# Kernel tuning notes

Hardware: AMD Instinct MI355X
Metric: run time of the kernel (lower is better)

The kernel has to match this reference:

```python
import jax, jax.numpy as jnp
import numpy as np

B, S, D, H = 4, 2048, 256, 8
DH = D // H  # d_head = 32


def setup_inputs() -> dict:
    key = jax.random.key(0)
    ks = jax.random.split(key, 7)
    scale = 1.0 / np.sqrt(D)  # ~ torch Linear init range
    sequences = jax.random.normal(ks[0], (B, S, D), dtype=jnp.float32)
    Wq = jax.random.uniform(ks[1], (H, D, DH), jnp.float32, -scale, scale)
    Wk = jax.random.uniform(ks[2], (H, D, DH), jnp.float32, -scale, scale)
    Wv = jax.random.uniform(ks[3], (H, D, DH), jnp.float32, -scale, scale)
    bq = jax.random.uniform(ks[4], (H, DH), jnp.float32, -scale, scale)
    bk = jax.random.uniform(ks[5], (H, DH), jnp.float32, -scale, scale)
    bv = jax.random.uniform(ks[6], (H, DH), jnp.float32, -scale, scale)
    return {"sequences": sequences, "Wq": Wq, "Wk": Wk, "Wv": Wv,
            "bq": bq, "bk": bk, "bv": bv}


def reference(sequences, Wq, Wk, Wv, bq, bk, bv):
    # Per-head linear maps of the FULL token (use_linear_mapping=True):
    # q[b,h,s,e] = sequences[b,s,:] @ Wq[h] + bq[h]
    q = jnp.einsum('bsd,hde->bhse', sequences, Wq) + bq[None, :, None, :]
    k = jnp.einsum('bsd,hde->bhse', sequences, Wk) + bk[None, :, None, :]
    v = jnp.einsum('bsd,hde->bhse', sequences, Wv) + bv[None, :, None, :]
    # Scaled dot-product attention per batch/head (full SxS matrix, as original)
    scores = jnp.einsum('bhse,bhte->bhst', q, k) / jnp.sqrt(jnp.float32(DH))
    attn = jax.nn.softmax(scores, axis=-1)
    out = jnp.einsum('bhst,bhte->bhse', attn, v)
    # hstack heads along feature dim -> [B, S, D]
    return out.transpose(0, 2, 1, 3).reshape(B, S, D)
```

## Files before the change

### kernel.cpp

```cpp
#include <hip/hip_runtime.h>
#include <hip/hip_bf16.h>


#define NB 4
#define NS 2048
#define ND 256
#define NH 8
#define NDH 32
#define KT 128
#define NT (NS / KT)

typedef __attribute__((ext_vector_type(8))) short short8;
typedef __attribute__((ext_vector_type(4))) float float4v;

static __device__ __forceinline__ unsigned short f2bf(float f) {
    union { float f; unsigned int u; } v; v.f = f;
    unsigned int r = (v.u + 0x7FFFu + ((v.u >> 16) & 1u)) >> 16;
    return (unsigned short)r;
}

static __device__ __forceinline__ unsigned int pk2bf(float lo, float hi) {
    __hip_bfloat162 h = __float22bfloat162_rn(float2{lo, hi});
    union { __hip_bfloat162 h; unsigned int u; } c; c.h = h;
    return c.u;
}

#if defined(__has_builtin)
#if __has_builtin(__builtin_amdgcn_exp2f)
#define EXP2F(x) __builtin_amdgcn_exp2f(x)
#endif
#endif
#ifndef EXP2F
#define EXP2F(x) exp2f(x)
#endif

#define SWZ(x) ((x) ^ ((((x) >> 7) & 7) << 4))

__global__ __launch_bounds__(256) void prep(const float* __restrict__ seq,
                                            unsigned short* __restrict__ seqb,
                                            const float* __restrict__ Wq,
                                            const float* __restrict__ Wk,
                                            const float* __restrict__ Wv,
                                            unsigned short* __restrict__ Wt) {
    int bx = (int)blockIdx.x;
    if (bx < 2048) {
        int i = (bx * 256 + (int)threadIdx.x) * 4;
        float4 v = *(const float4*)(seq + i);
        ushort4 o;
        o.x = f2bf(v.x); o.y = f2bf(v.y); o.z = f2bf(v.z); o.w = f2bf(v.w);
        *(ushort4*)(seqb + i) = o;
    } else {
        int idx = (bx - 2048) * 256 + (int)threadIdx.x;
        int c = idx >> 8, d = idx & 255;
        int mat = c >> 8;
        int cm = c & 255;
        int h = cm >> 5, e = cm & 31;
        const float* W = (mat == 0) ? Wq : (mat == 1) ? Wk : Wv;
        Wt[c * 256 + d] = f2bf(W[(h * 256 + d) * 32 + e]);
    }
}

__global__ __launch_bounds__(256, 2) void proj(const unsigned short* __restrict__ seqb,
                                               const unsigned short* __restrict__ Wt,
                                               const float* __restrict__ bq,
                                               const float* __restrict__ bk,
                                               const float* __restrict__ bv,
                                               unsigned short* __restrict__ Q,
                                               unsigned short* __restrict__ K,
                                               unsigned short* __restrict__ Vt) {
    __shared__ __align__(16) unsigned short plds[32768];

    int m0 = blockIdx.x * 64;
    int c0 = blockIdx.y * 64;
    int tid = (int)threadIdx.x;
    int wave = tid >> 6, lane = tid & 63;
    int g = lane >> 4, r4 = lane & 15;

#pragma unroll
    for (int j = 0; j < 16; ++j) {
        int s = tid + 256 * j;
        int local = s & 2047;
        int row = local >> 5;
        int col16 = (local & 31) ^ (row & 7);
        const unsigned short* src = (s < 2048)
            ? (seqb + (size_t)(m0 + row) * 256 + col16 * 8)
            : (Wt + (size_t)(c0 + row) * 256 + col16 * 8);
        __builtin_amdgcn_global_load_lds(
            (const __attribute__((address_space(1))) unsigned int*)src,
            (__attribute__((address_space(3))) unsigned int*)(&plds[s * 8]), 16, 0, 0);
    }
    __syncthreads();

    const unsigned short* ldsA = plds;
    const unsigned short* ldsB = plds + 16384;
    int rowA = wave * 16 + r4;
    int xA = r4 & 7;

    float4v acc[4];
#pragma unroll
    for (int ct = 0; ct < 4; ++ct) acc[ct] = (float4v){0.f, 0.f, 0.f, 0.f};

#pragma unroll
    for (int i = 0; i < 8; ++i) {
        int cp = ((4 * i + g) ^ xA) * 8;
        short8 a = *(const short8*)(ldsA + rowA * 256 + cp);
#pragma unroll
        for (int ct = 0; ct < 4; ++ct) {
            short8 b = *(const short8*)(ldsB + (ct * 16 + r4) * 256 + cp);
            acc[ct] = __builtin_amdgcn_mfma_f32_16x16x32_bf16(a, b, acc[ct], 0, 0, 0);
        }
    }

    const float SC = 0.17677669529663687f * 1.4426950408889634f;
#pragma unroll
    for (int ct = 0; ct < 4; ++ct) {
        int c = c0 + ct * 16 + r4;
        int mat = c >> 8;
        int cm = c & 255;
        int h = cm >> 5, e = cm & 31;
        float bias = ((mat == 0) ? bq : (mat == 1) ? bk : bv)[cm];
#pragma unroll
        for (int r = 0; r < 4; ++r) {
            int m = m0 + wave * 16 + 4 * g + r;
            int b = m >> 11, s = m & 2047;
            float val = acc[ct][r] + bias;
            if (mat == 0) {
                Q[((b * NH + h) * NS + s) * NDH + e] = f2bf(val * SC);
            } else if (mat == 1) {
                K[((b * NH + h) * NS + s) * NDH + e] = f2bf(val);
            } else {
                Vt[((b * NH + h) * NDH + e) * NS + s] = f2bf(val);
            }
        }
    }
}

__global__ __launch_bounds__(256, 2) void attn_kernel(const unsigned short* __restrict__ Q,
                                                      const unsigned short* __restrict__ K,
                                                      const unsigned short* __restrict__ Vt,
                                                      float* __restrict__ out) {
    __shared__ __align__(16) unsigned short lds[3][8192];

    int bx = (int)blockIdx.x;
    int wid = (bx & 7) * 64 + (bx >> 3);
    int bh = wid >> 4;
    int qt = wid & 15;
    int tid = (int)threadIdx.x;
    int wave = tid >> 6, lane = tid & 63;
    int g = lane >> 4, r4 = lane & 15;
    int q0 = qt * 128 + wave * 32;

    const unsigned short* Qb = Q + (size_t)bh * NS * NDH;
    const unsigned short* Kb = K + (size_t)bh * NS * NDH;
    const unsigned short* Vb = Vt + (size_t)bh * NDH * NS;

    const unsigned short* sgp;
    int strideT;
    int strideB;
    unsigned int sloff;
    {
        int slot = tid & 127;
        int sL = slot ^ ((slot >> 3) & 7);
        int row = sL >> 2, c16 = sL & 3;
        if (tid < 128) {
            int key = (row < 16) ? (2 * row) : (2 * (row - 16) + 1);
            sgp = Kb + key * NDH + c16 * 8;
            strideT = KT * NDH;
            strideB = 32 * NDH;
            sloff = slot * 8;
        } else {
            sgp = Vb + row * NS + c16 * 8;
            strideT = KT;
            strideB = 32;
            sloff = 1024 + slot * 8;
        }
    }

#define STAGE(bufi, t)                                                                        \
    do {                                                                                      \
        const unsigned short* _s = sgp + (size_t)(t) * strideT;                               \
        __builtin_amdgcn_global_load_lds(                                                     \
            (const __attribute__((address_space(1))) unsigned int*)(_s),                      \
            (__attribute__((address_space(3))) unsigned int*)(&lds[bufi][sloff]), 16, 0, 0);  \
        __builtin_amdgcn_global_load_lds(                                                     \
            (const __attribute__((address_space(1))) unsigned int*)(_s + strideB),            \
            (__attribute__((address_space(3))) unsigned int*)(&lds[bufi][sloff + 2048]), 16, 0, 0); \
        __builtin_amdgcn_global_load_lds(                                                     \
            (const __attribute__((address_space(1))) unsigned int*)(_s + 2 * strideB),        \
            (__attribute__((address_space(3))) unsigned int*)(&lds[bufi][sloff + 4096]), 16, 0, 0); \
        __builtin_amdgcn_global_load_lds(                                                     \
            (const __attribute__((address_space(1))) unsigned int*)(_s + 3 * strideB),        \
            (__attribute__((address_space(3))) unsigned int*)(&lds[bufi][sloff + 6144]), 16, 0, 0); \
    } while (0)

    int kOff0 = SWZ(r4 * 64 + g * 16);
    int kOff1 = SWZ((16 + r4) * 64 + g * 16);
    int vOff0 = 2048 + SWZ(r4 * 64 + g * 16);
    int vOff1 = 2048 + SWZ((16 + r4) * 64 + g * 16);

    short8 qf0 = *(const short8*)(Qb + (q0 + r4) * NDH + 8 * g);
    short8 qf1 = *(const short8*)(Qb + (q0 + 16 + r4) * NDH + 8 * g);

    const short ONE = (short)0x3F80;
    const short8 ones = {ONE, ONE, ONE, ONE, ONE, ONE, ONE, ONE};

    float4v aA0e = {0,0,0,0}, aB0e = {0,0,0,0}, aA1e = {0,0,0,0}, aB1e = {0,0,0,0};
    float4v aA0o = {0,0,0,0}, aB0o = {0,0,0,0}, aA1o = {0,0,0,0}, aB1o = {0,0,0,0};
    float4v lc0e = {0,0,0,0}, lc1e = {0,0,0,0}, lc0o = {0,0,0,0}, lc1o = {0,0,0,0};
    const float4v zero = {0.f, 0.f, 0.f, 0.f};

    auto process = [&](const char* buf, float4v& A0, float4v& B0, float4v& L0,
                       float4v& A1, float4v& B1, float4v& L1) {
        short8 kf0 = *(const short8*)(buf + kOff0);
        short8 kf1 = *(const short8*)(buf + kOff1);
        short8 va0 = *(const short8*)(buf + vOff0);
        short8 va1 = *(const short8*)(buf + vOff1);
        {
            float4v s0 = __builtin_amdgcn_mfma_f32_16x16x32_bf16(kf0, qf0, zero, 0, 0, 0);
            float4v s1 = __builtin_amdgcn_mfma_f32_16x16x32_bf16(kf1, qf0, zero, 0, 0, 0);
            union { short8 s; unsigned int u[4]; } pb;
#pragma unroll
            for (int r = 0; r < 4; ++r)
                pb.u[r] = pk2bf(EXP2F(s0[r]), EXP2F(s1[r]));
            A0 = __builtin_amdgcn_mfma_f32_16x16x32_bf16(va0, pb.s, A0, 0, 0, 0);
            B0 = __builtin_amdgcn_mfma_f32_16x16x32_bf16(va1, pb.s, B0, 0, 0, 0);
            L0 = __builtin_amdgcn_mfma_f32_16x16x32_bf16(ones, pb.s, L0, 0, 0, 0);
        }
        {
            float4v s0 = __builtin_amdgcn_mfma_f32_16x16x32_bf16(kf0, qf1, zero, 0, 0, 0);
            float4v s1 = __builtin_amdgcn_mfma_f32_16x16x32_bf16(kf1, qf1, zero, 0, 0, 0);
            union { short8 s; unsigned int u[4]; } pb;
#pragma unroll
            for (int r = 0; r < 4; ++r)
                pb.u[r] = pk2bf(EXP2F(s0[r]), EXP2F(s1[r]));
            A1 = __builtin_amdgcn_mfma_f32_16x16x32_bf16(va0, pb.s, A1, 0, 0, 0);
            B1 = __builtin_amdgcn_mfma_f32_16x16x32_bf16(va1, pb.s, B1, 0, 0, 0);
            L1 = __builtin_amdgcn_mfma_f32_16x16x32_bf16(ones, pb.s, L1, 0, 0, 0);
        }
    };

    STAGE(0, 0);
    STAGE(1, 1);

    int cur = 0;
    for (int t = 0; t < NT; ++t) {
        __builtin_amdgcn_s_barrier();
        if (t + 2 < NT) {
            int fut = cur + 2; if (fut >= 3) fut -= 3;
            STAGE(fut, t + 2);
            asm volatile("s_waitcnt vmcnt(8)" ::: "memory");
        } else if (t + 1 < NT) {
            asm volatile("s_waitcnt vmcnt(4)" ::: "memory");
        } else {
            asm volatile("s_waitcnt vmcnt(0)" ::: "memory");
        }
        __builtin_amdgcn_sched_barrier(0);

        __builtin_amdgcn_s_setprio(1);
        const char* buf = (const char*)lds[cur];
        process(buf,         aA0e, aB0e, lc0e, aA1e, aB1e, lc1e);
        process(buf + 4096,  aA0o, aB0o, lc0o, aA1o, aB1o, lc1o);
        process(buf + 8192,  aA0e, aB0e, lc0e, aA1e, aB1e, lc1e);
        process(buf + 12288, aA0o, aB0o, lc0o, aA1o, aB1o, lc1o);
        __builtin_amdgcn_s_setprio(0);

        __builtin_amdgcn_sched_barrier(0);
        ++cur; if (cur >= 3) cur -= 3;
    }

    float4v accA0 = aA0e + aA0o, accB0 = aB0e + aB0o;
    float4v accA1 = aA1e + aA1o, accB1 = aB1e + aB1o;
    float linv0 = 1.0f / (lc0e[0] + lc0o[0]);
    float linv1 = 1.0f / (lc1e[0] + lc1o[0]);

    int b = bh >> 3, h = bh & 7;
    {
        int s = q0 + r4;
        float* op = out + (size_t)(b * NS + s) * ND + h * NDH;
        float4 oa = {accA0[0] * linv0, accA0[1] * linv0, accA0[2] * linv0, accA0[3] * linv0};
        float4 ob = {accB0[0] * linv0, accB0[1] * linv0, accB0[2] * linv0, accB0[3] * linv0};
        *(float4*)(op + 4 * g) = oa;
        *(float4*)(op + 16 + 4 * g) = ob;
    }
    {
        int s = q0 + 16 + r4;
        float* op = out + (size_t)(b * NS + s) * ND + h * NDH;
        float4 oa = {accA1[0] * linv1, accA1[1] * linv1, accA1[2] * linv1, accA1[3] * linv1};
        float4 ob = {accB1[0] * linv1, accB1[1] * linv1, accB1[2] * linv1, accB1[3] * linv1};
        *(float4*)(op + 4 * g) = oa;
        *(float4*)(op + 16 + 4 * g) = ob;
    }
#undef STAGE
}

extern "C" void kernel_launch(void* const* d_in, const int* in_sizes, int n_in,
                              void* d_out, int out_size, void* d_ws, size_t ws_size,
                              hipStream_t stream) {
    const float* seq = (const float*)d_in[0];
    const float* Wq = (const float*)d_in[1];
    const float* Wk = (const float*)d_in[2];
    const float* Wv = (const float*)d_in[3];
    const float* bq = (const float*)d_in[4];
    const float* bk = (const float*)d_in[5];
    const float* bv = (const float*)d_in[6];
    float* out = (float*)d_out;

    unsigned short* seqb = (unsigned short*)d_ws;
    unsigned short* Wt = seqb + 2097152;
    unsigned short* Qw = Wt + 196608;
    unsigned short* Kw = Qw + 2097152;
    unsigned short* Vtw = Kw + 2097152;

    hipLaunchKernelGGL(prep, dim3(2816), dim3(256), 0, stream, seq, seqb, Wq, Wk, Wv, Wt);
    hipLaunchKernelGGL(proj, dim3(128, 12), dim3(256), 0, stream, seqb, Wt, bq, bk, bv, Qw, Kw, Vtw);
    hipLaunchKernelGGL(attn_kernel, dim3(512), dim3(256), 0, stream, Qw, Kw, Vtw, out);
}
```

Baseline: 57.05 us.

## Interleave LDS prefetch with compute and replace ones-MFMA row sums with VALU sums

The attention loop now waits for the current tile and then barriers, instead of barriering first and issuing all four global-to-LDS prefetches up front. The four prefetch loads for the tile two steps ahead are spread between the four process calls so they overlap the MFMA work. The softmax denominator is no longer computed with extra MFMAs against a ones matrix. Each lane sums the fp32 exponentials directly and reduces across lanes with shuffles at the end, which removes two MFMAs per process call but adds VALU adds and a different (fp32 rather than bf16-rounded) normalizer.

```diff
diff --git a/kernel.cpp b/kernel.cpp
--- a/kernel.cpp
+++ b/kernel.cpp
@@ -176,22 +176,10 @@
         }
     }
 
-#define STAGE(bufi, t)                                                                        \
-    do {                                                                                      \
-        const unsigned short* _s = sgp + (size_t)(t) * strideT;                               \
-        __builtin_amdgcn_global_load_lds(                                                     \
-            (const __attribute__((address_space(1))) unsigned int*)(_s),                      \
-            (__attribute__((address_space(3))) unsigned int*)(&lds[bufi][sloff]), 16, 0, 0);  \
-        __builtin_amdgcn_global_load_lds(                                                     \
-            (const __attribute__((address_space(1))) unsigned int*)(_s + strideB),            \
-            (__attribute__((address_space(3))) unsigned int*)(&lds[bufi][sloff + 2048]), 16, 0, 0); \
-        __builtin_amdgcn_global_load_lds(                                                     \
-            (const __attribute__((address_space(1))) unsigned int*)(_s + 2 * strideB),        \
-            (__attribute__((address_space(3))) unsigned int*)(&lds[bufi][sloff + 4096]), 16, 0, 0); \
-        __builtin_amdgcn_global_load_lds(                                                     \
-            (const __attribute__((address_space(1))) unsigned int*)(_s + 3 * strideB),        \
-            (__attribute__((address_space(3))) unsigned int*)(&lds[bufi][sloff + 6144]), 16, 0, 0); \
-    } while (0)
+#define STAGE1(bufi, t, p)                                                                    \
+    __builtin_amdgcn_global_load_lds(                                                         \
+        (const __attribute__((address_space(1))) unsigned int*)(sgp + (size_t)(t) * strideT + (p) * strideB), \
+        (__attribute__((address_space(3))) unsigned int*)(&lds[bufi][sloff + (p) * 2048]), 16, 0, 0)
 
     int kOff0 = SWZ(r4 * 64 + g * 16);
     int kOff1 = SWZ((16 + r4) * 64 + g * 16);
@@ -201,16 +189,12 @@
     short8 qf0 = *(const short8*)(Qb + (q0 + r4) * NDH + 8 * g);
     short8 qf1 = *(const short8*)(Qb + (q0 + 16 + r4) * NDH + 8 * g);
 
-    const short ONE = (short)0x3F80;
-    const short8 ones = {ONE, ONE, ONE, ONE, ONE, ONE, ONE, ONE};
-
     float4v aA0e = {0,0,0,0}, aB0e = {0,0,0,0}, aA1e = {0,0,0,0}, aB1e = {0,0,0,0};
     float4v aA0o = {0,0,0,0}, aB0o = {0,0,0,0}, aA1o = {0,0,0,0}, aB1o = {0,0,0,0};
-    float4v lc0e = {0,0,0,0}, lc1e = {0,0,0,0}, lc0o = {0,0,0,0}, lc1o = {0,0,0,0};
+    float l0 = 0.f, l1 = 0.f;
     const float4v zero = {0.f, 0.f, 0.f, 0.f};
 
-    auto process = [&](const char* buf, float4v& A0, float4v& B0, float4v& L0,
-                       float4v& A1, float4v& B1, float4v& L1) {
+    auto process = [&](const char* buf, float4v& A0, float4v& B0, float4v& A1, float4v& B1) {
         short8 kf0 = *(const short8*)(buf + kOff0);
         short8 kf1 = *(const short8*)(buf + kOff1);
         short8 va0 = *(const short8*)(buf + vOff0);
@@ -220,58 +204,67 @@
             float4v s1 = __builtin_amdgcn_mfma_f32_16x16x32_bf16(kf1, qf0, zero, 0, 0, 0);
             union { short8 s; unsigned int u[4]; } pb;
 #pragma unroll
-            for (int r = 0; r < 4; ++r)
-                pb.u[r] = pk2bf(EXP2F(s0[r]), EXP2F(s1[r]));
+            for (int r = 0; r < 4; ++r) {
+                float pe = EXP2F(s0[r]), po = EXP2F(s1[r]);
+                l0 += pe + po;
+                pb.u[r] = pk2bf(pe, po);
+            }
             A0 = __builtin_amdgcn_mfma_f32_16x16x32_bf16(va0, pb.s, A0, 0, 0, 0);
             B0 = __builtin_amdgcn_mfma_f32_16x16x32_bf16(va1, pb.s, B0, 0, 0, 0);
-            L0 = __builtin_amdgcn_mfma_f32_16x16x32_bf16(ones, pb.s, L0, 0, 0, 0);
         }
         {
             float4v s0 = __builtin_amdgcn_mfma_f32_16x16x32_bf16(kf0, qf1, zero, 0, 0, 0);
             float4v s1 = __builtin_amdgcn_mfma_f32_16x16x32_bf16(kf1, qf1, zero, 0, 0, 0);
             union { short8 s; unsigned int u[4]; } pb;
 #pragma unroll
-            for (int r = 0; r < 4; ++r)
-                pb.u[r] = pk2bf(EXP2F(s0[r]), EXP2F(s1[r]));
+            for (int r = 0; r < 4; ++r) {
+                float pe = EXP2F(s0[r]), po = EXP2F(s1[r]);
+                l1 += pe + po;
+                pb.u[r] = pk2bf(pe, po);
+            }
             A1 = __builtin_amdgcn_mfma_f32_16x16x32_bf16(va0, pb.s, A1, 0, 0, 0);
             B1 = __builtin_amdgcn_mfma_f32_16x16x32_bf16(va1, pb.s, B1, 0, 0, 0);
-            L1 = __builtin_amdgcn_mfma_f32_16x16x32_bf16(ones, pb.s, L1, 0, 0, 0);
         }
     };
 
-    STAGE(0, 0);
-    STAGE(1, 1);
+#pragma unroll
+    for (int p = 0; p < 4; ++p) STAGE1(0, 0, p);
+#pragma unroll
+    for (int p = 0; p < 4; ++p) STAGE1(1, 1, p);
 
     int cur = 0;
     for (int t = 0; t < NT; ++t) {
-        __builtin_amdgcn_s_barrier();
-        if (t + 2 < NT) {
-            int fut = cur + 2; if (fut >= 3) fut -= 3;
-            STAGE(fut, t + 2);
-            asm volatile("s_waitcnt vmcnt(8)" ::: "memory");
-        } else if (t + 1 < NT) {
+        if (t + 1 < NT) {
             asm volatile("s_waitcnt vmcnt(4)" ::: "memory");
         } else {
             asm volatile("s_waitcnt vmcnt(0)" ::: "memory");
         }
         __builtin_amdgcn_sched_barrier(0);
+        __builtin_amdgcn_s_barrier();
+
+        int fut = cur + 2; if (fut >= 3) fut -= 3;
+        bool stg = (t + 2 < NT);
+        const char* buf = (const char*)lds[cur];
 
         __builtin_amdgcn_s_setprio(1);
-        const char* buf = (const char*)lds[cur];
-        process(buf,         aA0e, aB0e, lc0e, aA1e, aB1e, lc1e);
-        process(buf + 4096,  aA0o, aB0o, lc0o, aA1o, aB1o, lc1o);
-        process(buf + 8192,  aA0e, aB0e, lc0e, aA1e, aB1e, lc1e);
-        process(buf + 12288, aA0o, aB0o, lc0o, aA1o, aB1o, lc1o);
+        if (stg) STAGE1(fut, t + 2, 0);
+        process(buf,         aA0e, aB0e, aA1e, aB1e);
+        if (stg) STAGE1(fut, t + 2, 1);
+        process(buf + 4096,  aA0o, aB0o, aA1o, aB1o);
+        if (stg) STAGE1(fut, t + 2, 2);
+        process(buf + 8192,  aA0e, aB0e, aA1e, aB1e);
+        if (stg) STAGE1(fut, t + 2, 3);
+        process(buf + 12288, aA0o, aB0o, aA1o, aB1o);
         __builtin_amdgcn_s_setprio(0);
 
-        __builtin_amdgcn_sched_barrier(0);
         ++cur; if (cur >= 3) cur -= 3;
     }
 
     float4v accA0 = aA0e + aA0o, accB0 = aB0e + aB0o;
     float4v accA1 = aA1e + aA1o, accB1 = aB1e + aB1o;
-    float linv0 = 1.0f / (lc0e[0] + lc0o[0]);
-    float linv1 = 1.0f / (lc1e[0] + lc1o[0]);
+    l0 += __shfl_xor(l0, 16); l0 += __shfl_xor(l0, 32);
+    l1 += __shfl_xor(l1, 16); l1 += __shfl_xor(l1, 32);
+    float linv0 = 1.0f / l0, linv1 = 1.0f / l1;
 
     int b = bh >> 3, h = bh & 7;
     {
@@ -290,7 +283,7 @@
         *(float4*)(op + 4 * g) = oa;
         *(float4*)(op + 16 + 4 * g) = ob;
     }
-#undef STAGE
+#undef STAGE1
 }
 
 extern "C" void kernel_launch(void* const* d_in, const int* in_sizes, int n_in,
```

Result: slower. 58.34 us (+2.3%).

## Switch attention inner loop to 32x32x16 MFMA with VALU row-sum

Applied to the files above, without the earlier changes.

Replaces the 16x16x32 bf16 MFMA tiling with 32x32x16 MFMAs, so each wave computes a 32-query by 32-key score block and a 32x32 output tile directly. The row-sum denominator now comes from VALU adds of the exponentials plus a cross-half shuffle, replacing the extra MFMA against a vector of ones. The LDS staging layout and swizzle are rewritten to match the new fragment shapes. The aim is fewer MFMA issues and less instruction overhead per tile, at the cost of more VALU work and a riskier layout remap.

```diff
diff --git a/kernel.cpp b/kernel.cpp
--- a/kernel.cpp
+++ b/kernel.cpp
@@ -12,6 +12,7 @@
 
 typedef __attribute__((ext_vector_type(8))) short short8;
 typedef __attribute__((ext_vector_type(4))) float float4v;
+typedef __attribute__((ext_vector_type(16))) float float16v;
 
 static __device__ __forceinline__ unsigned short f2bf(float f) {
     union { float f; unsigned int u; } v; v.f = f;
@@ -33,8 +34,6 @@
 #ifndef EXP2F
 #define EXP2F(x) exp2f(x)
 #endif
-
-#define SWZ(x) ((x) ^ ((((x) >> 7) & 7) << 4))
 
 __global__ __launch_bounds__(256) void prep(const float* __restrict__ seq,
                                             unsigned short* __restrict__ seqb,
@@ -147,7 +146,7 @@
     int qt = wid & 15;
     int tid = (int)threadIdx.x;
     int wave = tid >> 6, lane = tid & 63;
-    int g = lane >> 4, r4 = lane & 15;
+    int r31 = lane & 31, hi2 = lane >> 5;
     int q0 = qt * 128 + wave * 32;
 
     const unsigned short* Qb = Q + (size_t)bh * NS * NDH;
@@ -159,20 +158,20 @@
     int strideB;
     unsigned int sloff;
     {
-        int slot = tid & 127;
-        int sL = slot ^ ((slot >> 3) & 7);
-        int row = sL >> 2, c16 = sL & 3;
+        int s = tid & 127;
+        int row = s >> 2;
+        int srcC = (s & 3) ^ ((row >> 1) & 3);
         if (tid < 128) {
-            int key = (row < 16) ? (2 * row) : (2 * (row - 16) + 1);
-            sgp = Kb + key * NDH + c16 * 8;
+            int key = (row & ~12) | ((row & 4) << 1) | ((row & 8) >> 1);
+            sgp = Kb + key * NDH + srcC * 8;
             strideT = KT * NDH;
             strideB = 32 * NDH;
-            sloff = slot * 8;
+            sloff = s * 8;
         } else {
-            sgp = Vb + row * NS + c16 * 8;
+            sgp = Vb + row * NS + srcC * 8;
             strideT = KT;
             strideB = 32;
-            sloff = 1024 + slot * 8;
+            sloff = 1024 + s * 8;
         }
     }
 
@@ -193,50 +192,40 @@
             (__attribute__((address_space(3))) unsigned int*)(&lds[bufi][sloff + 6144]), 16, 0, 0); \
     } while (0)
 
-    int kOff0 = SWZ(r4 * 64 + g * 16);
-    int kOff1 = SWZ((16 + r4) * 64 + g * 16);
-    int vOff0 = 2048 + SWZ(r4 * 64 + g * 16);
-    int vOff1 = 2048 + SWZ((16 + r4) * 64 + g * 16);
-
-    short8 qf0 = *(const short8*)(Qb + (q0 + r4) * NDH + 8 * g);
-    short8 qf1 = *(const short8*)(Qb + (q0 + 16 + r4) * NDH + 8 * g);
-
-    const short ONE = (short)0x3F80;
-    const short8 ones = {ONE, ONE, ONE, ONE, ONE, ONE, ONE, ONE};
-
-    float4v aA0e = {0,0,0,0}, aB0e = {0,0,0,0}, aA1e = {0,0,0,0}, aB1e = {0,0,0,0};
-    float4v aA0o = {0,0,0,0}, aB0o = {0,0,0,0}, aA1o = {0,0,0,0}, aB1o = {0,0,0,0};
-    float4v lc0e = {0,0,0,0}, lc1e = {0,0,0,0}, lc0o = {0,0,0,0}, lc1o = {0,0,0,0};
-    const float4v zero = {0.f, 0.f, 0.f, 0.f};
-
-    auto process = [&](const char* buf, float4v& A0, float4v& B0, float4v& L0,
-                       float4v& A1, float4v& B1, float4v& L1) {
-        short8 kf0 = *(const short8*)(buf + kOff0);
-        short8 kf1 = *(const short8*)(buf + kOff1);
-        short8 va0 = *(const short8*)(buf + vOff0);
-        short8 va1 = *(const short8*)(buf + vOff1);
-        {
-            float4v s0 = __builtin_amdgcn_mfma_f32_16x16x32_bf16(kf0, qf0, zero, 0, 0, 0);
-            float4v s1 = __builtin_amdgcn_mfma_f32_16x16x32_bf16(kf1, qf0, zero, 0, 0, 0);
-            union { short8 s; unsigned int u[4]; } pb;
-#pragma unroll
-            for (int r = 0; r < 4; ++r)
-                pb.u[r] = pk2bf(EXP2F(s0[r]), EXP2F(s1[r]));
-            A0 = __builtin_amdgcn_mfma_f32_16x16x32_bf16(va0, pb.s, A0, 0, 0, 0);
-            B0 = __builtin_amdgcn_mfma_f32_16x16x32_bf16(va1, pb.s, B0, 0, 0, 0);
-            L0 = __builtin_amdgcn_mfma_f32_16x16x32_bf16(ones, pb.s, L0, 0, 0, 0);
-        }
-        {
-            float4v s0 = __builtin_amdgcn_mfma_f32_16x16x32_bf16(kf0, qf1, zero, 0, 0, 0);
-            float4v s1 = __builtin_amdgcn_mfma_f32_16x16x32_bf16(kf1, qf1, zero, 0, 0, 0);
-            union { short8 s; unsigned int u[4]; } pb;
-#pragma unroll
-            for (int r = 0; r < 4; ++r)
-                pb.u[r] = pk2bf(EXP2F(s0[r]), EXP2F(s1[r]));
-            A1 = __builtin_amdgcn_mfma_f32_16x16x32_bf16(va0, pb.s, A1, 0, 0, 0);
-            B1 = __builtin_amdgcn_mfma_f32_16x16x32_bf16(va1, pb.s, B1, 0, 0, 0);
-            L1 = __builtin_amdgcn_mfma_f32_16x16x32_bf16(ones, pb.s, L1, 0, 0, 0);
-        }
+    int rx = (r31 >> 1) & 3;
+    int kOffA = r31 * 64 + ((hi2 ^ rx) << 4);
+    int kOffB = r31 * 64 + (((2 + hi2) ^ rx) << 4);
+    int vOffA = 2048 + r31 * 64 + ((hi2 ^ rx) << 4);
+    int vOffB = 2048 + r31 * 64 + (((2 + hi2) ^ rx) << 4);
+
+    const unsigned short* qrow = Qb + (q0 + r31) * NDH;
+    short8 qa = *(const short8*)(qrow + 8 * hi2);
+    short8 qb = *(const short8*)(qrow + 16 + 8 * hi2);
+
+    float16v accE = {0.f}, accO = {0.f};
+    const float16v zero16 = {0.f};
+    float lp = 0.f;
+
+    auto process = [&](const char* buf, float16v& acc) {
+        short8 kfA = *(const short8*)(buf + kOffA);
+        short8 kfB = *(const short8*)(buf + kOffB);
+        short8 vfA = *(const short8*)(buf + vOffA);
+        short8 vfB = *(const short8*)(buf + vOffB);
+        float16v s = __builtin_amdgcn_mfma_f32_32x32x16_bf16(kfA, qa, zero16, 0, 0, 0);
+        s = __builtin_amdgcn_mfma_f32_32x32x16_bf16(kfB, qb, s, 0, 0, 0);
+        float p[16];
+#pragma unroll
+        for (int r = 0; r < 16; ++r) p[r] = EXP2F(s[r]);
+#pragma unroll
+        for (int r = 0; r < 16; ++r) lp += p[r];
+        union { short8 v; unsigned int u[4]; } pb1, pb2;
+#pragma unroll
+        for (int w = 0; w < 4; ++w) {
+            pb1.u[w] = pk2bf(p[2 * w], p[2 * w + 1]);
+            pb2.u[w] = pk2bf(p[8 + 2 * w], p[9 + 2 * w]);
+        }
+        acc = __builtin_amdgcn_mfma_f32_32x32x16_bf16(vfA, pb1.v, acc, 0, 0, 0);
+        acc = __builtin_amdgcn_mfma_f32_32x32x16_bf16(vfB, pb2.v, acc, 0, 0, 0);
     };
 
     STAGE(0, 0);
@@ -258,37 +247,28 @@
 
         __builtin_amdgcn_s_setprio(1);
         const char* buf = (const char*)lds[cur];
-        process(buf,         aA0e, aB0e, lc0e, aA1e, aB1e, lc1e);
-        process(buf + 4096,  aA0o, aB0o, lc0o, aA1o, aB1o, lc1o);
-        process(buf + 8192,  aA0e, aB0e, lc0e, aA1e, aB1e, lc1e);
-        process(buf + 12288, aA0o, aB0o, lc0o, aA1o, aB1o, lc1o);
+        process(buf, accE);
+        process(buf + 4096, accO);
+        process(buf + 8192, accE);
+        process(buf + 12288, accO);
         __builtin_amdgcn_s_setprio(0);
 
         __builtin_amdgcn_sched_barrier(0);
         ++cur; if (cur >= 3) cur -= 3;
     }
 
-    float4v accA0 = aA0e + aA0o, accB0 = aB0e + aB0o;
-    float4v accA1 = aA1e + aA1o, accB1 = aB1e + aB1o;
-    float linv0 = 1.0f / (lc0e[0] + lc0o[0]);
-    float linv1 = 1.0f / (lc1e[0] + lc1o[0]);
+    lp += __shfl_xor(lp, 32);
+    float linv = 1.0f / lp;
+    float16v accT = accE + accO;
 
     int b = bh >> 3, h = bh & 7;
-    {
-        int s = q0 + r4;
-        float* op = out + (size_t)(b * NS + s) * ND + h * NDH;
-        float4 oa = {accA0[0] * linv0, accA0[1] * linv0, accA0[2] * linv0, accA0[3] * linv0};
-        float4 ob = {accB0[0] * linv0, accB0[1] * linv0, accB0[2] * linv0, accB0[3] * linv0};
-        *(float4*)(op + 4 * g) = oa;
-        *(float4*)(op + 16 + 4 * g) = ob;
-    }
-    {
-        int s = q0 + 16 + r4;
-        float* op = out + (size_t)(b * NS + s) * ND + h * NDH;
-        float4 oa = {accA1[0] * linv1, accA1[1] * linv1, accA1[2] * linv1, accA1[3] * linv1};
-        float4 ob = {accB1[0] * linv1, accB1[1] * linv1, accB1[2] * linv1, accB1[3] * linv1};
-        *(float4*)(op + 4 * g) = oa;
-        *(float4*)(op + 16 + 4 * g) = ob;
+    int srow = q0 + r31;
+    float* op = out + (size_t)(b * NS + srow) * ND + h * NDH + 4 * hi2;
+#pragma unroll
+    for (int i = 0; i < 4; ++i) {
+        float4 o4 = {accT[4 * i] * linv, accT[4 * i + 1] * linv,
+                     accT[4 * i + 2] * linv, accT[4 * i + 3] * linv};
+        *(float4*)(op + 8 * i) = o4;
     }
 #undef STAGE
 }
```

New measurement: 58.23 us. 2.1% more time.
